# Optimization experiments

Hardware: AMD Instinct MI355X
Metric: run time of the kernel (lower is better)

The kernel has to match this reference:

```python
import jax, jax.numpy as jnp
import numpy as np
import math

DIM = 1024
ATTN_DIM = 1024
B, S = 2, 4096

def setup_inputs() -> dict:
    key = jax.random.key(0)
    k1, k2, k3 = jax.random.split(key, 3)
    x = jax.random.normal(k1, (B, S, DIM), dtype=jnp.float32)
    # qkv Linear(dim, 3*attn_dim, bias=True): weight [3*attn_dim, dim], bias [3*attn_dim]
    W_qkv = jax.random.normal(k2, (3 * ATTN_DIM, DIM), dtype=jnp.float32) * (1.0 / math.sqrt(DIM))
    b_qkv = jax.random.normal(k3, (3 * ATTN_DIM,), dtype=jnp.float32) * 0.01
    return {"x": x, "W_qkv": W_qkv, "b_qkv": b_qkv}

def reference(x, W_qkv, b_qkv):
    b, s, d = x.shape
    qkv = jnp.einsum('bsd,ed->bse', x, W_qkv) + b_qkv  # [B,S,3*attn_dim]
    q, k, v = jnp.split(qkv, 3, axis=-1)
    score = jnp.einsum('bqd,bkd->bqk', q, k)  # [B,S,S]
    # causal mask applied BEFORE scaling (matches original: -inf survives the divide)
    causal = jnp.tril(jnp.ones((s, s), dtype=bool))
    score = jnp.where(causal, score, -jnp.inf)
    attn = jax.nn.softmax(score / math.sqrt(ATTN_DIM), axis=-1)
    y = jnp.einsum('bqk,bkd->bqd', attn, v)  # [B,S,attn_dim]
    return y
```

## Files before the change

kernel.cpp:

```cpp
#include <hip/hip_runtime.h>
#include <cstdint>
#include <cstddef>

typedef __bf16 bf16;
typedef bf16 bf16x4 __attribute__((ext_vector_type(4)));
typedef bf16 bf16x8 __attribute__((ext_vector_type(8)));
typedef float f32x4 __attribute__((ext_vector_type(4)));

#define SEQ 4096
#define DIMD 1024

#define TILE_K1024 131072L
#define TILE_K4096 524288L

__device__ __forceinline__ void async16(void* lds, const void* g) {
    __builtin_amdgcn_global_load_lds(
        (__attribute__((address_space(1))) void*)g,
        (__attribute__((address_space(3))) void*)lds,
        16, 0, 0);
}

__device__ __forceinline__ void gemm_core(
    const bf16* __restrict__ At, const bf16* __restrict__ Bt,
    int k0, int k1, f32x4 acc[4][4])
{
    __shared__ bf16 lA[4096];
    __shared__ bf16 lB[4096];
    const int tid  = threadIdx.x;
    const int lane = tid & 63;
    const int wid  = tid >> 6;
    const int wm   = (wid >> 1) * 64;
    const int wn   = (wid & 1) * 64;
    const int lr   = lane & 15;
    const int kq   = (lane >> 4) * 8;

    for (int kk = k0; kk < k1; ++kk) {
        const bf16* sa = At + (long)kk * 4096;
        const bf16* sb = Bt + (long)kk * 4096;
        async16(&lA[tid * 8],        sa + tid * 8);
        async16(&lA[2048 + tid * 8], sa + 2048 + tid * 8);
        async16(&lB[tid * 8],        sb + tid * 8);
        async16(&lB[2048 + tid * 8], sb + 2048 + tid * 8);
        __syncthreads();

        bf16x8 af[4], bfr[4];
#pragma unroll
        for (int mi = 0; mi < 4; ++mi)
            af[mi] = *(const bf16x8*)&lA[(wm + mi * 16 + lr) * 32 + kq];
#pragma unroll
        for (int ni = 0; ni < 4; ++ni)
            bfr[ni] = *(const bf16x8*)&lB[(wn + ni * 16 + lr) * 32 + kq];
#pragma unroll
        for (int mi = 0; mi < 4; ++mi)
#pragma unroll
            for (int ni = 0; ni < 4; ++ni)
                acc[mi][ni] = __builtin_amdgcn_mfma_f32_16x16x32_bf16(
                    af[mi], bfr[ni], acc[mi][ni], 0, 0, 0);
        __syncthreads();
    }
}

__global__ __launch_bounds__(256) void cvt_tile_kernel(const float* __restrict__ in,
                                                       bf16* __restrict__ out, int n4)
{
    const int i = blockIdx.x * 256 + threadIdx.x;
    if (i >= n4) return;
    const float4 v = ((const float4*)in)[i];
    const int j = i * 4, row = j >> 10, col = j & 1023;
    const long o = (long)(row >> 7) * TILE_K1024 + (col >> 5) * 4096
                 + (row & 127) * 32 + (col & 31);
    bf16x4 ov = { (bf16)v.x, (bf16)v.y, (bf16)v.z, (bf16)v.w };
    *(bf16x4*)&out[o] = ov;
}

__global__ __launch_bounds__(256) void zero_kernel(float* __restrict__ p)
{
    p[blockIdx.x * 256 + threadIdx.x] = 0.0f;
}

__global__ __launch_bounds__(256) void qkv_gemm(
    const bf16* __restrict__ xt, const bf16* __restrict__ wt,
    const float* __restrict__ bias,
    bf16* __restrict__ Qt, bf16* __restrict__ Kt, bf16* __restrict__ Vtt)
{
    const int bm = blockIdx.y * 128, bn = blockIdx.x * 128;
    f32x4 acc[4][4] = {};
    gemm_core(xt + (long)(bm >> 7) * TILE_K1024,
              wt + (long)(bn >> 7) * TILE_K1024, 0, 32, acc);

    const int tid = threadIdx.x, lane = tid & 63, wid = tid >> 6;
    const int wm = (wid >> 1) * 64, wn = (wid & 1) * 64;
    const int lr = lane & 15, q4 = (lane >> 4) * 4;
#pragma unroll
    for (int ni = 0; ni < 4; ++ni) {
        const int n = bn + wn + ni * 16 + lr;
        const float bv = bias[n];
#pragma unroll
        for (int mi = 0; mi < 4; ++mi) {
            const int m0 = bm + wm + mi * 16 + q4;
            if (n < 2048) {
                bf16* dst = (n < 1024) ? Qt : Kt;
                const int c = n & 1023;
#pragma unroll
                for (int r = 0; r < 4; ++r) {
                    const int m = m0 + r;
                    dst[(long)(m >> 7) * TILE_K1024 + (c >> 5) * 4096
                        + (m & 127) * 32 + (c & 31)] = (bf16)(acc[mi][ni][r] + bv);
                }
            } else {
                const int b = m0 >> 12, s = m0 & 4095, d = n - 2048;
                bf16x4 o = { (bf16)(acc[mi][ni][0] + bv), (bf16)(acc[mi][ni][1] + bv),
                             (bf16)(acc[mi][ni][2] + bv), (bf16)(acc[mi][ni][3] + bv) };
                *(bf16x4*)&Vtt[(long)b * 4194304 + (long)(d >> 7) * TILE_K4096
                               + (s >> 5) * 4096 + (d & 127) * 32 + (s & 31)] = o;
            }
        }
    }
}

__global__ __launch_bounds__(256) void score_kernel(
    const bf16* __restrict__ Qt, const bf16* __restrict__ Kt,
    bf16* __restrict__ P, long Pstride, float* __restrict__ sums, int batch0)
{
    const int i = blockIdx.x;
    int qt = (int)((sqrtf((float)(8 * i + 1)) - 1.0f) * 0.5f);
    while ((qt + 1) * (qt + 2) / 2 <= i) ++qt;
    while (qt * (qt + 1) / 2 > i) --qt;
    const int kt = i - qt * (qt + 1) / 2;

    const int bz = blockIdx.y, batch = batch0 + bz;
    bf16* Pb = P + (long)bz * Pstride;
    float* sb = sums + (long)batch * SEQ;

    f32x4 acc[4][4] = {};
    gemm_core(Qt + (long)(batch * 32 + qt) * TILE_K1024,
              Kt + (long)(batch * 32 + kt) * TILE_K1024, 0, 32, acc);

    const int tid = threadIdx.x, lane = tid & 63, wid = tid >> 6;
    const int wm = (wid >> 1) * 64, wn = (wid & 1) * 64;
    const int lr = lane & 15, q4 = (lane >> 4) * 4;
#pragma unroll
    for (int mi = 0; mi < 4; ++mi) {
#pragma unroll
        for (int r = 0; r < 4; ++r) {
            const int ql = wm + mi * 16 + q4 + r;
            const int q  = qt * 128 + ql;
            float rsum = 0.0f;
#pragma unroll
            for (int ni = 0; ni < 4; ++ni) {
                const int key = kt * 128 + wn + ni * 16 + lr;
                const float s = acc[mi][ni][r] * 0.03125f;
                const float p = (key <= q) ? __expf(s) : 0.0f;
                const bf16 pb = (bf16)p;
                Pb[(long)qt * TILE_K4096 + (key >> 5) * 4096 + ql * 32 + (key & 31)] = pb;
                rsum += (float)pb;
            }
            rsum += __shfl_xor(rsum, 1);
            rsum += __shfl_xor(rsum, 2);
            rsum += __shfl_xor(rsum, 4);
            rsum += __shfl_xor(rsum, 8);
            if (lr == 0) atomicAdd(&sb[q], rsum);
        }
    }
}

__global__ __launch_bounds__(256) void pv_kernel(
    const bf16* __restrict__ P, long Pstride, const bf16* __restrict__ Vtt,
    const float* __restrict__ sums, float* __restrict__ Y,
    float* __restrict__ Ypart, int batch0)
{
    const int y = blockIdx.y, dt = blockIdx.x;
    const bool tail = (y >= 32);
    int qt;
    if (!tail) qt = (y & 1) ? (31 - (y >> 1)) : (y >> 1);
    else { const int t = y - 32; qt = 16 + ((t & 1) ? (15 - (t >> 1)) : (t >> 1)); }
    const int ext = (qt + 1) * 4;
    const int k0 = tail ? 64 : 0;
    const int k1 = tail ? ext : (ext < 64 ? ext : 64);

    const int bz = blockIdx.z, batch = batch0 + bz;
    const bf16* Pb = P + (long)bz * Pstride;
    const float* sb = sums + (long)batch * SEQ;

    f32x4 acc[4][4] = {};
    gemm_core(Pb + (long)qt * TILE_K4096,
              Vtt + (long)batch * 4194304 + (long)dt * TILE_K4096, k0, k1, acc);

    const int tid = threadIdx.x, lane = tid & 63, wid = tid >> 6;
    const int wm = (wid >> 1) * 64, wn = (wid & 1) * 64;
    const int lr = lane & 15, q4 = (lane >> 4) * 4;
#pragma unroll
    for (int mi = 0; mi < 4; ++mi) {
#pragma unroll
        for (int r = 0; r < 4; ++r) {
            const int q = qt * 128 + wm + mi * 16 + q4 + r;
            const float iv = 1.0f / sb[q];
#pragma unroll
            for (int ni = 0; ni < 4; ++ni) {
                const int d = dt * 128 + wn + ni * 16 + lr;
                const float v = acc[mi][ni][r] * iv;
                if (!tail) Y[(long)batch * 4194304 + (long)q * DIMD + d] = v;
                else Ypart[(long)batch * 2097152 + (long)(q - 2048) * DIMD + d] = v;
            }
        }
    }
}

__global__ __launch_bounds__(256) void combine_kernel(float* __restrict__ Y,
                                                      const float* __restrict__ Ypart)
{
    const int i = blockIdx.x * 256 + threadIdx.x;
    const long j = (long)i * 4;
    const int b = (int)(j >> 21);
    const long rem = j & 2097151;
    float4 a = *(const float4*)&Y[(long)b * 4194304 + 2097152 + rem];
    const float4 p = *(const float4*)&Ypart[(long)b * 2097152 + rem];
    a.x += p.x; a.y += p.y; a.z += p.z; a.w += p.w;
    *(float4*)&Y[(long)b * 4194304 + 2097152 + rem] = a;
}

extern "C" void kernel_launch(void* const* d_in, const int* in_sizes, int n_in,
                              void* d_out, int out_size, void* d_ws, size_t ws_size,
                              hipStream_t stream)
{
    const float* x    = (const float*)d_in[0];
    const float* W    = (const float*)d_in[1];
    const float* bqkv = (const float*)d_in[2];
    float* out = (float*)d_out;
    char* ws = (char*)d_ws;

    const size_t MB = 1024 * 1024;
    const bool par = ws_size >= (size_t)112 * MB + 64 * 1024;

    const size_t base = par ? 64 * MB : 32 * MB;
    bf16* P0   = (bf16*)ws;
    bf16* xt   = (bf16*)ws;
    bf16* wt   = (bf16*)(ws + 16 * MB);
    bf16* Qt   = (bf16*)(ws + base);
    bf16* Kt   = (bf16*)(ws + base + 16 * MB);
    bf16* Vtt  = (bf16*)(ws + base + 32 * MB);
    float* sums  = (float*)(ws + base + 48 * MB);
    float* Ypart = (float*)(ws + base);

    const long PSTR = (long)SEQ * SEQ;

    cvt_tile_kernel<<<8192, 256, 0, stream>>>(x, xt, 8192 * 1024 / 4);
    cvt_tile_kernel<<<3072, 256, 0, stream>>>(W, wt, 3072 * 1024 / 4);
    zero_kernel<<<32, 256, 0, stream>>>(sums);
    qkv_gemm<<<dim3(24, 64), 256, 0, stream>>>(xt, wt, bqkv, Qt, Kt, Vtt);

    if (par) {
        score_kernel<<<dim3(528, 2), 256, 0, stream>>>(Qt, Kt, P0, PSTR, sums, 0);
        pv_kernel<<<dim3(8, 48, 2), 256, 0, stream>>>(P0, PSTR, Vtt, sums, out, Ypart, 0);
    } else {
        for (int b = 0; b < 2; ++b) {
            score_kernel<<<dim3(528, 1), 256, 0, stream>>>(Qt, Kt, P0, 0, sums, b);
            pv_kernel<<<dim3(8, 48, 1), 256, 0, stream>>>(P0, 0, Vtt, sums, out, Ypart, b);
        }
    }
    combine_kernel<<<4096, 256, 0, stream>>>(out, Ypart);
}
```

Measured before the change: 286.0 us.

## Compact causal P storage, XCD-aware block mapping, and balanced split-K PV schedule

```diff
diff --git a/kernel.cpp b/kernel.cpp
--- a/kernel.cpp
+++ b/kernel.cpp
@@ -9,9 +9,9 @@
 
 #define SEQ 4096
 #define DIMD 1024
-
 #define TILE_K1024 131072L
 #define TILE_K4096 524288L
+#define PC_BATCH   8650752L
 
 __device__ __forceinline__ void async16(void* lds, const void* g) {
     __builtin_amdgcn_global_load_lds(
@@ -60,11 +60,15 @@
     }
 }
 
-__global__ __launch_bounds__(256) void cvt_tile_kernel(const float* __restrict__ in,
-                                                       bf16* __restrict__ out, int n4)
-{
-    const int i = blockIdx.x * 256 + threadIdx.x;
-    if (i >= n4) return;
+__global__ __launch_bounds__(256) void cvt_all_kernel(
+    const float* __restrict__ x, const float* __restrict__ W,
+    bf16* __restrict__ xt, bf16* __restrict__ wt, float* __restrict__ sums)
+{
+    const int g = blockIdx.x, tid = threadIdx.x;
+    if (g >= 11264) { sums[(g - 11264) * 256 + tid] = 0.0f; return; }
+    const float* in; bf16* out; int i;
+    if (g < 8192) { in = x; out = xt; i = g * 256 + tid; }
+    else          { in = W; out = wt; i = (g - 8192) * 256 + tid; }
     const float4 v = ((const float4*)in)[i];
     const int j = i * 4, row = j >> 10, col = j & 1023;
     const long o = (long)(row >> 7) * TILE_K1024 + (col >> 5) * 4096
@@ -73,20 +77,17 @@
     *(bf16x4*)&out[o] = ov;
 }
 
-__global__ __launch_bounds__(256) void zero_kernel(float* __restrict__ p)
-{
-    p[blockIdx.x * 256 + threadIdx.x] = 0.0f;
-}
-
 __global__ __launch_bounds__(256) void qkv_gemm(
     const bf16* __restrict__ xt, const bf16* __restrict__ wt,
     const float* __restrict__ bias,
     bf16* __restrict__ Qt, bf16* __restrict__ Kt, bf16* __restrict__ Vtt)
 {
-    const int bm = blockIdx.y * 128, bn = blockIdx.x * 128;
+    const int b = blockIdx.x, x = b & 7, r = b >> 3;
+    const int mt = x * 8 + r / 24, wnid = r % 24;
+    const int bm = mt * 128, bn = wnid * 128;
+
     f32x4 acc[4][4] = {};
-    gemm_core(xt + (long)(bm >> 7) * TILE_K1024,
-              wt + (long)(bn >> 7) * TILE_K1024, 0, 32, acc);
+    gemm_core(xt + (long)mt * TILE_K1024, wt + (long)wnid * TILE_K1024, 0, 32, acc);
 
     const int tid = threadIdx.x, lane = tid & 63, wid = tid >> 6;
     const int wm = (wid >> 1) * 64, wn = (wid & 1) * 64;
@@ -102,16 +103,16 @@
                 bf16* dst = (n < 1024) ? Qt : Kt;
                 const int c = n & 1023;
 #pragma unroll
-                for (int r = 0; r < 4; ++r) {
-                    const int m = m0 + r;
+                for (int rr = 0; rr < 4; ++rr) {
+                    const int m = m0 + rr;
                     dst[(long)(m >> 7) * TILE_K1024 + (c >> 5) * 4096
-                        + (m & 127) * 32 + (c & 31)] = (bf16)(acc[mi][ni][r] + bv);
+                        + (m & 127) * 32 + (c & 31)] = (bf16)(acc[mi][ni][rr] + bv);
                 }
             } else {
-                const int b = m0 >> 12, s = m0 & 4095, d = n - 2048;
+                const int bb = m0 >> 12, s = m0 & 4095, d = n - 2048;
                 bf16x4 o = { (bf16)(acc[mi][ni][0] + bv), (bf16)(acc[mi][ni][1] + bv),
                              (bf16)(acc[mi][ni][2] + bv), (bf16)(acc[mi][ni][3] + bv) };
-                *(bf16x4*)&Vtt[(long)b * 4194304 + (long)(d >> 7) * TILE_K4096
+                *(bf16x4*)&Vtt[(long)bb * 4194304 + (long)(d >> 7) * TILE_K4096
                                + (s >> 5) * 4096 + (d & 127) * 32 + (s & 31)] = o;
             }
         }
@@ -120,16 +121,20 @@
 
 __global__ __launch_bounds__(256) void score_kernel(
     const bf16* __restrict__ Qt, const bf16* __restrict__ Kt,
-    bf16* __restrict__ P, long Pstride, float* __restrict__ sums, int batch0)
-{
-    const int i = blockIdx.x;
-    int qt = (int)((sqrtf((float)(8 * i + 1)) - 1.0f) * 0.5f);
-    while ((qt + 1) * (qt + 2) / 2 <= i) ++qt;
-    while (qt * (qt + 1) / 2 > i) --qt;
-    const int kt = i - qt * (qt + 1) / 2;
-
-    const int bz = blockIdx.y, batch = batch0 + bz;
-    bf16* Pb = P + (long)bz * Pstride;
+    bf16* __restrict__ Pc, float* __restrict__ sums, int batch0)
+{
+    const int b = blockIdx.x, x = b & 7;
+    int r = b >> 3;
+    const int batch = batch0 + r / 66, bz = r / 66;
+    r %= 66;
+    int qt, kt;
+    const int s0 = x + 1;
+    if (r < s0)           { qt = x;      kt = r; }
+    else if (r < 33)      { qt = 31 - x; kt = r - s0; }
+    else if (r < 42 + x)  { qt = x + 8;  kt = r - 33; }
+    else                  { qt = 23 - x; kt = r - 42 - x; }
+
+    bf16* Pb = Pc + (long)bz * PC_BATCH + (long)(qt * (qt + 1) / 2 + kt) * 16384;
     float* sb = sums + (long)batch * SEQ;
 
     f32x4 acc[4][4] = {};
@@ -142,17 +147,18 @@
 #pragma unroll
     for (int mi = 0; mi < 4; ++mi) {
 #pragma unroll
-        for (int r = 0; r < 4; ++r) {
-            const int ql = wm + mi * 16 + q4 + r;
+        for (int rr = 0; rr < 4; ++rr) {
+            const int ql = wm + mi * 16 + q4 + rr;
             const int q  = qt * 128 + ql;
             float rsum = 0.0f;
 #pragma unroll
             for (int ni = 0; ni < 4; ++ni) {
-                const int key = kt * 128 + wn + ni * 16 + lr;
-                const float s = acc[mi][ni][r] * 0.03125f;
+                const int kl  = wn + ni * 16 + lr;
+                const int key = kt * 128 + kl;
+                const float s = acc[mi][ni][rr] * 0.03125f;
                 const float p = (key <= q) ? __expf(s) : 0.0f;
                 const bf16 pb = (bf16)p;
-                Pb[(long)qt * TILE_K4096 + (key >> 5) * 4096 + ql * 32 + (key & 31)] = pb;
+                Pb[(kl >> 5) * 4096 + ql * 32 + (kl & 31)] = pb;
                 rsum += (float)pb;
             }
             rsum += __shfl_xor(rsum, 1);
@@ -164,26 +170,63 @@
     }
 }
 
+__global__ __launch_bounds__(128) void schedule_kernel(int* __restrict__ cnt,
+                                                       int4* __restrict__ tab, int nb)
+{
+    __shared__ short sz[128];
+    __shared__ int m0[128], mk[128];
+    __shared__ unsigned char sorted[128];
+    const int t = threadIdx.x, G = 62 * nb;
+    if (t < G) {
+        const int gp = t % 62, bz = t / 62;
+        int qt, c;
+        if (gp < 10)      { qt = gp;                 c = 0; }
+        else if (gp < 38) { qt = 10 + (gp - 10) / 2; c = (gp - 10) & 1; }
+        else              { qt = 24 + (gp - 38) / 3; c = (gp - 38) % 3; }
+        const int nc = qt < 10 ? 1 : (qt < 24 ? 2 : 3);
+        const int ext = (qt + 1) * 4;
+        const int k0 = ext * c / nc, k1 = ext * (c + 1) / nc;
+        sz[t] = (short)(k1 - k0);
+        m0[t] = qt | (bz << 8) | (c << 16);
+        mk[t] = k0 | (k1 << 16);
+    }
+    __syncthreads();
+    if (t < G) {
+        int rank = 0; const short mys = sz[t];
+        for (int j = 0; j < G; ++j) {
+            const short s = sz[j];
+            if (s > mys || (s == mys && j < t)) ++rank;
+        }
+        sorted[rank] = (unsigned char)t;
+    }
+    __syncthreads();
+    if (t == 0) {
+        int fill[8] = {0, 0, 0, 0, 0, 0, 0, 0};
+        for (int r = 0; r < G; ++r) {
+            const int x = ((r >> 3) & 1) ? 7 - (r & 7) : (r & 7);
+            const int g = sorted[r];
+            tab[x * 16 + fill[x]++] = make_int4(m0[g], mk[g] & 0xffff, mk[g] >> 16, 0);
+        }
+        for (int x = 0; x < 8; ++x) cnt[x] = fill[x];
+    }
+}
+
 __global__ __launch_bounds__(256) void pv_kernel(
-    const bf16* __restrict__ P, long Pstride, const bf16* __restrict__ Vtt,
-    const float* __restrict__ sums, float* __restrict__ Y,
-    float* __restrict__ Ypart, int batch0)
-{
-    const int y = blockIdx.y, dt = blockIdx.x;
-    const bool tail = (y >= 32);
-    int qt;
-    if (!tail) qt = (y & 1) ? (31 - (y >> 1)) : (y >> 1);
-    else { const int t = y - 32; qt = 16 + ((t & 1) ? (15 - (t >> 1)) : (t >> 1)); }
-    const int ext = (qt + 1) * 4;
-    const int k0 = tail ? 64 : 0;
-    const int k1 = tail ? ext : (ext < 64 ? ext : 64);
-
-    const int bz = blockIdx.z, batch = batch0 + bz;
-    const bf16* Pb = P + (long)bz * Pstride;
-    const float* sb = sums + (long)batch * SEQ;
+    const bf16* __restrict__ Pc, const bf16* __restrict__ Vtt,
+    const float* __restrict__ sums, const int* __restrict__ cnt,
+    const int4* __restrict__ tab, float* __restrict__ Y,
+    float* __restrict__ slot0, float* __restrict__ slot1, int batch0)
+{
+    const int b = blockIdx.x, x = b & 7, t = b >> 3;
+    const int j = t >> 3, dt = t & 7;
+    if (j >= cnt[x]) return;
+    const int4 e = tab[x * 16 + j];
+    const int qt = e.x & 255, bz = (e.x >> 8) & 255, slot = (e.x >> 16) & 255;
+    const int k0 = e.y, k1 = e.z;
+    const int batch = batch0 + bz;
 
     f32x4 acc[4][4] = {};
-    gemm_core(Pb + (long)qt * TILE_K4096,
+    gemm_core(Pc + (long)bz * PC_BATCH + (long)(qt * (qt + 1) / 2) * 16384,
               Vtt + (long)batch * 4194304 + (long)dt * TILE_K4096, k0, k1, acc);
 
     const int tid = threadIdx.x, lane = tid & 63, wid = tid >> 6;
@@ -192,31 +235,42 @@
 #pragma unroll
     for (int mi = 0; mi < 4; ++mi) {
 #pragma unroll
-        for (int r = 0; r < 4; ++r) {
-            const int q = qt * 128 + wm + mi * 16 + q4 + r;
-            const float iv = 1.0f / sb[q];
+        for (int rr = 0; rr < 4; ++rr) {
+            const int q = qt * 128 + wm + mi * 16 + q4 + rr;
+            const float iv = 1.0f / sums[(long)batch * SEQ + q];
 #pragma unroll
             for (int ni = 0; ni < 4; ++ni) {
                 const int d = dt * 128 + wn + ni * 16 + lr;
-                const float v = acc[mi][ni][r] * iv;
-                if (!tail) Y[(long)batch * 4194304 + (long)q * DIMD + d] = v;
-                else Ypart[(long)batch * 2097152 + (long)(q - 2048) * DIMD + d] = v;
+                const float v = acc[mi][ni][rr] * iv;
+                if (slot == 0)
+                    Y[(long)batch * 4194304 + (long)q * DIMD + d] = v;
+                else if (slot == 1)
+                    slot0[((long)bz * 2816 + (q - 1280)) * DIMD + d] = v;
+                else
+                    slot1[((long)bz * 1024 + (q - 3072)) * DIMD + d] = v;
             }
         }
     }
 }
 
-__global__ __launch_bounds__(256) void combine_kernel(float* __restrict__ Y,
-                                                      const float* __restrict__ Ypart)
-{
-    const int i = blockIdx.x * 256 + threadIdx.x;
-    const long j = (long)i * 4;
-    const int b = (int)(j >> 21);
-    const long rem = j & 2097151;
-    float4 a = *(const float4*)&Y[(long)b * 4194304 + 2097152 + rem];
-    const float4 p = *(const float4*)&Ypart[(long)b * 2097152 + rem];
-    a.x += p.x; a.y += p.y; a.z += p.z; a.w += p.w;
-    *(float4*)&Y[(long)b * 4194304 + 2097152 + rem] = a;
+__global__ __launch_bounds__(256) void combine_kernel(
+    float* __restrict__ Y, const float* __restrict__ slot0,
+    const float* __restrict__ slot1, int batch0)
+{
+    const long g = (long)blockIdx.x * 256 + threadIdx.x;
+    const long e4 = g * 4;
+    const int bz = (int)(e4 / 2883584);
+    const long rem = e4 % 2883584;
+    const int q = 1280 + (int)(rem >> 10), d = (int)(rem & 1023);
+    const int batch = batch0 + bz;
+    float4 a = *(const float4*)&Y[(long)batch * 4194304 + (long)q * DIMD + d];
+    const float4 p0 = *(const float4*)&slot0[e4];
+    a.x += p0.x; a.y += p0.y; a.z += p0.z; a.w += p0.w;
+    if (q >= 3072) {
+        const float4 p1 = *(const float4*)&slot1[((long)bz * 1024 + (q - 3072)) * DIMD + d];
+        a.x += p1.x; a.y += p1.y; a.z += p1.z; a.w += p1.w;
+    }
+    *(float4*)&Y[(long)batch * 4194304 + (long)q * DIMD + d] = a;
 }
 
 extern "C" void kernel_launch(void* const* d_in, const int* in_sizes, int n_in,
@@ -229,34 +283,48 @@
     float* out = (float*)d_out;
     char* ws = (char*)d_ws;
 
-    const size_t MB = 1024 * 1024;
-    const bool par = ws_size >= (size_t)112 * MB + 64 * 1024;
-
-    const size_t base = par ? 64 * MB : 32 * MB;
-    bf16* P0   = (bf16*)ws;
-    bf16* xt   = (bf16*)ws;
-    bf16* wt   = (bf16*)(ws + 16 * MB);
-    bf16* Qt   = (bf16*)(ws + base);
-    bf16* Kt   = (bf16*)(ws + base + 16 * MB);
-    bf16* Vtt  = (bf16*)(ws + base + 32 * MB);
-    float* sums  = (float*)(ws + base + 48 * MB);
-    float* Ypart = (float*)(ws + base);
-
-    const long PSTR = (long)SEQ * SEQ;
-
-    cvt_tile_kernel<<<8192, 256, 0, stream>>>(x, xt, 8192 * 1024 / 4);
-    cvt_tile_kernel<<<3072, 256, 0, stream>>>(W, wt, 3072 * 1024 / 4);
-    zero_kernel<<<32, 256, 0, stream>>>(sums);
-    qkv_gemm<<<dim3(24, 64), 256, 0, stream>>>(xt, wt, bqkv, Qt, Kt, Vtt);
-
+    const size_t MiB = 1024 * 1024;
+    const size_t PAR_REQ = 84934656 + 32768 + 64 + 2048 + 1024;
+    const bool par = ws_size >= PAR_REQ;
+
+    bf16 *Pc, *xt, *wt, *Qt, *Kt, *Vtt;
+    float *sums, *slot0, *slot1;
+    int* cnt; int4* tab;
     if (par) {
-        score_kernel<<<dim3(528, 2), 256, 0, stream>>>(Qt, Kt, P0, PSTR, sums, 0);
-        pv_kernel<<<dim3(8, 48, 2), 256, 0, stream>>>(P0, PSTR, Vtt, sums, out, Ypart, 0);
+        Pc = (bf16*)ws; xt = (bf16*)ws; wt = (bf16*)(ws + 16 * MiB);
+        Qt = (bf16*)(ws + 34603008); Kt = (bf16*)(ws + 34603008 + 16 * MiB);
+        Vtt = (bf16*)(ws + 34603008 + 32 * MiB);
+        sums = (float*)(ws + 84934656);
+        cnt  = (int*)(ws + 84934656 + 32768);
+        tab  = (int4*)(ws + 84934656 + 32768 + 64);
+        slot0 = (float*)Qt;
+        slot1 = (float*)((char*)Qt + 23068672);
+    } else {
+        Pc = (bf16*)ws; xt = (bf16*)ws;
+        Qt = (bf16*)(ws + 17301504); Kt = (bf16*)(ws + 17301504 + 16 * MiB);
+        Vtt = (bf16*)(ws + 17301504 + 32 * MiB);
+        sums = (float*)(ws + 67633152);
+        cnt  = (int*)(ws + 67633152 + 32768);
+        tab  = (int4*)(ws + 67633152 + 32768 + 64);
+        wt   = (bf16*)(ws + 67698688);
+        slot0 = (float*)Qt;
+        slot1 = (float*)((char*)Qt + 11534336);
+    }
+
+    cvt_all_kernel<<<11296, 256, 0, stream>>>(x, W, xt, wt, sums);
+    qkv_gemm<<<1536, 256, 0, stream>>>(xt, wt, bqkv, Qt, Kt, Vtt);
+
+    if (par) {
+        schedule_kernel<<<1, 128, 0, stream>>>(cnt, tab, 2);
+        score_kernel<<<1056, 256, 0, stream>>>(Qt, Kt, Pc, sums, 0);
+        pv_kernel<<<1024, 256, 0, stream>>>(Pc, Vtt, sums, cnt, tab, out, slot0, slot1, 0);
+        combine_kernel<<<5632, 256, 0, stream>>>(out, slot0, slot1, 0);
     } else {
         for (int b = 0; b < 2; ++b) {
-            score_kernel<<<dim3(528, 1), 256, 0, stream>>>(Qt, Kt, P0, 0, sums, b);
-            pv_kernel<<<dim3(8, 48, 1), 256, 0, stream>>>(P0, 0, Vtt, sums, out, Ypart, b);
-        }
-    }
-    combine_kernel<<<4096, 256, 0, stream>>>(out, Ypart);
-}
+            schedule_kernel<<<1, 128, 0, stream>>>(cnt, tab, 1);
+            score_kernel<<<528, 256, 0, stream>>>(Qt, Kt, Pc, sums, b);
+            pv_kernel<<<1024, 256, 0, stream>>>(Pc, Vtt, sums, cnt, tab, out, slot0, slot1, b);
+            combine_kernel<<<2816, 256, 0, stream>>>(out, slot0, slot1, b);
+        }
+    }
+}
```

Result: slower. 304.5 us (+6.4%).
